# Kernel tuning notes

Hardware: AMD Instinct MI355X
Metric: run time of the kernel (lower is better)

The kernel has to match this reference:

```python
import jax, jax.numpy as jnp
import numpy as np

B, S, D = 1, 2048, 2048
H, G = 32, 8            # n_heads, n_groups
HPG = H // G            # heads per group = 4
HD = D // H             # head_dim = 64


def setup_inputs() -> dict:
    key = jax.random.key(0)
    ks = jax.random.split(key, 5)
    w_scale = 0.02
    return {
        "x":  jax.random.normal(ks[0], (B, S, D), dtype=jnp.float32),
        "Wq": jax.random.normal(ks[1], (D, D), dtype=jnp.float32) * w_scale,
        "bq": jnp.zeros((D,), dtype=jnp.float32),
        "Wk": jax.random.normal(ks[2], (G * HD, D), dtype=jnp.float32) * w_scale,
        "bk": jnp.zeros((G * HD,), dtype=jnp.float32),
        "Wv": jax.random.normal(ks[3], (G * HD, D), dtype=jnp.float32) * w_scale,
        "bv": jnp.zeros((G * HD,), dtype=jnp.float32),
        "Wo": jax.random.normal(ks[4], (D, D), dtype=jnp.float32) * w_scale,
        "bo": jnp.zeros((D,), dtype=jnp.float32),
    }


def reference(x, Wq, bq, Wk, bk, Wv, bv, Wo, bo):
    b, n, _ = x.shape
    # projections (torch Linear: y = x @ W.T + b)
    q = x @ Wq.T + bq                              # [b, n, D]
    k = x @ Wk.T + bk                              # [b, n, G*HD]
    v = x @ Wv.T + bv                              # [b, n, G*HD]
    # q: [b, n, H, HD] -> [b, H, n, HD] -> split heads as (g h): [b, G, HPG, n, HD]
    q = q.reshape(b, n, H, HD).transpose(0, 2, 1, 3).reshape(b, G, HPG, n, HD)
    k = k.reshape(b, n, G, HD).transpose(0, 2, 1, 3)   # [b, G, n, HD]
    v = v.reshape(b, n, G, HD).transpose(0, 2, 1, 3)   # [b, G, n, HD]
    scale = 1.0 / jnp.sqrt(jnp.asarray(HD, dtype=q.dtype))
    attn_score = jnp.einsum('bghnd,bgsd->bghns', q, k) * scale
    attn_prob = jax.nn.softmax(attn_score, axis=-1)
    out = jnp.einsum('bghns,bgsd->bghnd', attn_prob, v)   # [b, G, HPG, n, HD]
    # faithful to original: rearrange 'b g h n d -> b n (h g d)' (h-major, g-minor)
    out = out.transpose(0, 3, 2, 1, 4).reshape(b, n, HPG * G * HD)
    return out @ Wo.T + bo
```

## Files before the change

kernel.cpp:

```cpp
#include <hip/hip_runtime.h>
#include <hip/hip_bf16.h>

constexpr int kS   = 2048;
constexpr int kD   = 2048;
constexpr int kG   = 8;
constexpr int kHD  = 64;
constexpr int kGHD = 512;
constexpr int kNQKV = kD + 2 * kGHD;

constexpr float kQScale = 0.125f * 1.4426950408889634f;

typedef __attribute__((ext_vector_type(8))) _Float16 f16x8;
typedef __attribute__((ext_vector_type(4))) float    f32x4;

__device__ __forceinline__ ushort f2h(float x) {
    return __builtin_bit_cast(ushort, (_Float16)x);
}
__device__ __forceinline__ float h2f(ushort u) {
    return (float)__builtin_bit_cast(_Float16, u);
}
__device__ __forceinline__ float fast_exp2(float x) {
    return __builtin_amdgcn_exp2f(x);
}

__global__ __launch_bounds__(256) void cvt_f16(
    const float* __restrict__ in, ushort* __restrict__ out, int n, float scale)
{
    const int i = (blockIdx.x * 256 + threadIdx.x) * 4;
    if (i >= n) return;
    const float4 x = *(const float4*)&in[i];
    ushort4 o;
    o.x = f2h(x.x * scale); o.y = f2h(x.y * scale);
    o.z = f2h(x.z * scale); o.w = f2h(x.w * scale);
    *(ushort4*)&out[i] = o;
}

__global__ __launch_bounds__(256) void prep_bias(
    const float* __restrict__ bq, const float* __restrict__ bk,
    const float* __restrict__ bv, float* __restrict__ bqkv)
{
    const int i = blockIdx.x * 256 + threadIdx.x;
    if (i < kD)             bqkv[i] = bq[i] * kQScale;
    else if (i < kD + kGHD) bqkv[i] = bk[i - kD];
    else if (i < kNQKV)     bqkv[i] = bv[i - kD - kGHD];
}

__device__ __forceinline__ int xcd_swizzle(int orig, int nwg) {
    const int cpx = nwg >> 3;
    return (orig & 7) * cpx + (orig >> 3);
}

#define GEMM_PRELUDE(Aptr, Bptr)                                              \
    const int bid  = xcd_swizzle(blockIdx.x, gridDim.x);                      \
    const int m0   = (bid / gridX) * 128;                                     \
    const int n0   = (bid % gridX) * 128;                                     \
    const int tid  = threadIdx.x;                                             \
    const int w    = tid >> 6;                                                \
    const int lane = tid & 63;                                                \
    const int wm   = w >> 2;                                                  \
    const int wn   = w & 3;                                                   \
    const int fr   = lane & 15;                                               \
    const int kq   = lane >> 4;                                               \
    const int srow = w * 16 + (lane >> 2);                                    \
    const int sslot = ((lane & 3) ^ ((lane >> 3) & 3)) * 8;                   \
    const ushort* gA = (Aptr) + (size_t)(m0 + srow) * K + sslot;              \
    const ushort* gB = (Bptr) + (size_t)(n0 + srow) * K + sslot;              \
    const int pslot = (kq ^ ((fr >> 1) & 3)) * 8;                             \
    f32x4 acc[4][2];                                                          \
    _Pragma("unroll")                                                         \
    for (int mi = 0; mi < 4; ++mi)                                            \
        _Pragma("unroll")                                                     \
        for (int ni = 0; ni < 2; ++ni) {                                      \
            f32x4 z = {0.f, 0.f, 0.f, 0.f};                                   \
            acc[mi][ni] = z;                                                  \
        }

#define GEMM_STAGE(buf, k0)                                                   \
    do {                                                                      \
        __builtin_amdgcn_global_load_lds(                                     \
            (const __attribute__((address_space(1))) void*)(gA + (k0)),       \
            (__attribute__((address_space(3))) void*)&lds[buf][0][w * 512],   \
            16, 0, 0);                                                        \
        __builtin_amdgcn_global_load_lds(                                     \
            (const __attribute__((address_space(1))) void*)(gB + (k0)),       \
            (__attribute__((address_space(3))) void*)&lds[buf][1][w * 512],   \
            16, 0, 0);                                                        \
    } while (0)

#define GEMM_KLOOP(MFMA_BODY)                                                 \
    GEMM_STAGE(0, 0);                                                         \
    __syncthreads();                                                          \
    int cur = 0;                                                              \
    for (int k0 = 0; k0 < K; k0 += 32) {                                      \
        if (k0 + 32 < K) GEMM_STAGE(cur ^ 1, k0 + 32);                        \
        f16x8 af[4], bf[2];                                                   \
        _Pragma("unroll")                                                     \
        for (int f = 0; f < 4; ++f)                                           \
            af[f] = *(const f16x8*)&lds[cur][0][(wm * 64 + f * 16 + fr) * 32 + pslot]; \
        _Pragma("unroll")                                                     \
        for (int f = 0; f < 2; ++f)                                           \
            bf[f] = *(const f16x8*)&lds[cur][1][(wn * 32 + f * 16 + fr) * 32 + pslot]; \
        __builtin_amdgcn_s_setprio(1);                                        \
        MFMA_BODY                                                             \
        __builtin_amdgcn_s_setprio(0);                                        \
        __syncthreads();                                                      \
        cur ^= 1;                                                             \
    }

__global__ __launch_bounds__(512) void gemm_qkv(
    const ushort* __restrict__ Af, const ushort* __restrict__ Bf,
    const float* __restrict__ bias,
    ushort* __restrict__ qb16, ushort* __restrict__ kb16, ushort* __restrict__ vt16,
    int K, int gridX)
{
    __shared__ ushort lds[2][2][128 * 32];

    GEMM_PRELUDE(Af, Bf)
    GEMM_KLOOP(
        _Pragma("unroll")
        for (int mi = 0; mi < 4; ++mi)
            _Pragma("unroll")
            for (int ni = 0; ni < 2; ++ni)
                acc[mi][ni] = __builtin_amdgcn_mfma_f32_16x16x32_f16(
                    af[mi], bf[ni], acc[mi][ni], 0, 0, 0);
    )

    const int seg = (n0 < kD) ? 0 : (n0 < kD + kGHD) ? 1 : 2;
    #pragma unroll
    for (int ni = 0; ni < 2; ++ni) {
        const int ncol = n0 + wn * 32 + ni * 16 + fr;
        const float bv = bias[ncol];
        #pragma unroll
        for (int mi = 0; mi < 4; ++mi) {
            #pragma unroll
            for (int i = 0; i < 4; ++i) {
                const int row = m0 + wm * 64 + mi * 16 + kq * 4 + i;
                const ushort u = f2h(acc[mi][ni][i] + bv);
                if (seg == 0)      qb16[(size_t)row * kD   + ncol]              = u;
                else if (seg == 1) kb16[(size_t)row * kGHD + (ncol - kD)]       = u;
                else               vt16[(size_t)(ncol - kD - kGHD) * kS + row]  = u;
            }
        }
    }
}

__global__ __launch_bounds__(512) void gemm_o(
    const ushort* __restrict__ Af, const ushort* __restrict__ Bf,
    const float* __restrict__ bias, float* __restrict__ C, int K, int N, int gridX)
{
    __shared__ ushort lds[2][2][128 * 32];

    GEMM_PRELUDE(Af, Bf)
    GEMM_KLOOP(
        _Pragma("unroll")
        for (int mi = 0; mi < 4; ++mi)
            _Pragma("unroll")
            for (int ni = 0; ni < 2; ++ni)
                acc[mi][ni] = __builtin_amdgcn_mfma_f32_16x16x32_f16(
                    af[mi], bf[ni], acc[mi][ni], 0, 0, 0);
    )

    #pragma unroll
    for (int ni = 0; ni < 2; ++ni) {
        const int ncol = n0 + wn * 32 + ni * 16 + fr;
        const float bv = bias[ncol];
        #pragma unroll
        for (int mi = 0; mi < 4; ++mi)
            #pragma unroll
            for (int i = 0; i < 4; ++i) {
                const int row = m0 + wm * 64 + mi * 16 + kq * 4 + i;
                C[(size_t)row * N + ncol] = acc[mi][ni][i] + bv;
            }
    }
}

__global__ __launch_bounds__(512) void gqa_attn_mfma(
    const ushort* __restrict__ qb,
    const ushort* __restrict__ kb,
    const ushort* __restrict__ vt,
    ushort* __restrict__ oh)
{
    __shared__ ushort Kt[2][64 * 64];
    __shared__ ushort Vt[2][64 * 64];
    __shared__ ushort Pt[8][16 * 64];

    const int g    = blockIdx.y;
    const int q0   = blockIdx.x * 32;
    const int tid  = threadIdx.x;
    const int w    = tid >> 6;
    const int lane = tid & 63;
    const int hp   = w & 3;
    const int qh   = w >> 2;
    const int fr   = lane & 15;
    const int lq   = lane >> 4;
    const int h    = g * 4 + hp;
    const int qbase = q0 + qh * 16;

    const int r = w * 8 + (lane >> 3);
    const int s = (lane & 7) ^ (r & 7);

    __builtin_amdgcn_global_load_lds(
        (const __attribute__((address_space(1))) void*)(kb + (size_t)r * kGHD + g * kHD + s * 8),
        (__attribute__((address_space(3))) void*)(Kt[0] + w * 512), 16, 0, 0);
    __builtin_amdgcn_global_load_lds(
        (const __attribute__((address_space(1))) void*)(vt + (size_t)(g * kHD + r) * kS + s * 8),
        (__attribute__((address_space(3))) void*)(Vt[0] + w * 512), 16, 0, 0);

    f16x8 qf[2];
    #pragma unroll
    for (int ks = 0; ks < 2; ++ks)
        qf[ks] = *(const f16x8*)&qb[(size_t)(qbase + fr) * kD + h * kHD + ks * 32 + lq * 8];

    float mrow = -1e30f, lrow = 0.f;

    f32x4 oacc[4];
    #pragma unroll
    for (int ni = 0; ni < 4; ++ni) {
        f32x4 z = {0.f, 0.f, 0.f, 0.f};
        oacc[ni] = z;
    }

    int cur = 0;
    for (int t = 0; t < kS; t += 64) {
        __syncthreads();

        if (t + 64 < kS) {
            __builtin_amdgcn_global_load_lds(
                (const __attribute__((address_space(1))) void*)
                    (kb + (size_t)(t + 64 + r) * kGHD + g * kHD + s * 8),
                (__attribute__((address_space(3))) void*)(Kt[cur ^ 1] + w * 512), 16, 0, 0);
            __builtin_amdgcn_global_load_lds(
                (const __attribute__((address_space(1))) void*)
                    (vt + (size_t)(g * kHD + r) * kS + t + 64 + s * 8),
                (__attribute__((address_space(3))) void*)(Vt[cur ^ 1] + w * 512), 16, 0, 0);
        }

        f32x4 sc[4];
        #pragma unroll
        for (int ni = 0; ni < 4; ++ni) {
            f32x4 z = {0.f, 0.f, 0.f, 0.f};
            sc[ni] = z;
        }
        #pragma unroll
        for (int ks = 0; ks < 2; ++ks) {
            f16x8 kf[4];
            #pragma unroll
            for (int ni = 0; ni < 4; ++ni)
                kf[ni] = *(const f16x8*)&Kt[cur][(ni * 16 + fr) * 64
                                                 + (((ks * 4 + lq) ^ (fr & 7)) * 8)];
            __builtin_amdgcn_s_setprio(1);
            #pragma unroll
            for (int ni = 0; ni < 4; ++ni)
                sc[ni] = __builtin_amdgcn_mfma_f32_16x16x32_f16(
                    kf[ni], qf[ks], sc[ni], 0, 0, 0);
            __builtin_amdgcn_s_setprio(0);
        }

        float mt = sc[0][0];
        #pragma unroll
        for (int ni = 0; ni < 4; ++ni)
            #pragma unroll
            for (int i = 0; i < 4; ++i)
                mt = fmaxf(mt, sc[ni][i]);
        mt = fmaxf(mt, __shfl_xor(mt, 16));
        mt = fmaxf(mt, __shfl_xor(mt, 32));

        if (__any(mt > mrow + 11.5f)) {
            const float mnew = (mt > mrow + 11.5f) ? mt : mrow;
            const float c = fast_exp2(mrow - mnew);
            lrow *= c;
            mrow = mnew;
            #pragma unroll
            for (int i = 0; i < 4; ++i) {
                const float ci = __shfl(c, lq * 4 + i);
                #pragma unroll
                for (int ni = 0; ni < 4; ++ni)
                    oacc[ni][i] *= ci;
            }
        }

        float ps = 0.f;
        #pragma unroll
        for (int ni = 0; ni < 4; ++ni)
            #pragma unroll
            for (int i = 0; i < 4; ++i) {
                const float p = fast_exp2(sc[ni][i] - mrow);
                sc[ni][i] = p;
                ps += p;
            }
        ps += __shfl_xor(ps, 16);
        ps += __shfl_xor(ps, 32);
        lrow += ps;

        #pragma unroll
        for (int ni = 0; ni < 4; ++ni) {
            const int kg0  = ni * 16 + lq * 4;
            const int slot = (kg0 >> 3) ^ (fr & 7);
            ushort4 pk;
            pk.x = f2h(sc[ni][0]); pk.y = f2h(sc[ni][1]);
            pk.z = f2h(sc[ni][2]); pk.w = f2h(sc[ni][3]);
            *(ushort4*)&Pt[w][fr * 64 + slot * 8 + (kg0 & 7)] = pk;
        }

        #pragma unroll
        for (int ks = 0; ks < 2; ++ks) {
            f16x8 pf, vf[4];
            pf = *(const f16x8*)&Pt[w][fr * 64 + (((ks * 4 + lq) ^ (fr & 7)) * 8)];
            #pragma unroll
            for (int ni = 0; ni < 4; ++ni)
                vf[ni] = *(const f16x8*)&Vt[cur][(ni * 16 + fr) * 64
                                                 + (((ks * 4 + lq) ^ (fr & 7)) * 8)];
            __builtin_amdgcn_s_setprio(1);
            #pragma unroll
            for (int ni = 0; ni < 4; ++ni)
                oacc[ni] = __builtin_amdgcn_mfma_f32_16x16x32_f16(
                    pf, vf[ni], oacc[ni], 0, 0, 0);
            __builtin_amdgcn_s_setprio(0);
        }
        cur ^= 1;
    }

    const float inv = 1.f / lrow;
    #pragma unroll
    for (int i = 0; i < 4; ++i) {
        const float invi = __shfl(inv, lq * 4 + i);
        const size_t row = qbase + lq * 4 + i;
        #pragma unroll
        for (int ni = 0; ni < 4; ++ni) {
            const float o = oacc[ni][i] * invi;
            const size_t addr = row * kD + hp * kGHD + g * kHD + ni * 16 + fr;
            oh[addr] = f2h(o);
        }
    }
}

extern "C" void kernel_launch(void* const* d_in, const int* in_sizes, int n_in,
                              void* d_out, int out_size, void* d_ws, size_t ws_size,
                              hipStream_t stream)
{
    const float* x  = (const float*)d_in[0];
    const float* Wq = (const float*)d_in[1];
    const float* bq = (const float*)d_in[2];
    const float* Wk = (const float*)d_in[3];
    const float* bk = (const float*)d_in[4];
    const float* Wv = (const float*)d_in[5];
    const float* bv = (const float*)d_in[6];
    const float* Wo = (const float*)d_in[7];
    const float* bo = (const float*)d_in[8];
    float* out = (float*)d_out;

    char* p = (char*)d_ws;
    ushort* xf    = (ushort*)p; p += (size_t)kS * kD * 2;
    ushort* wqkvf = (ushort*)p; p += (size_t)kNQKV * kD * 2;
    ushort* wof   = (ushort*)p; p += (size_t)kD * kD * 2;
    float*  bqkv  = (float*)p;  p += 16384;
    ushort* qb16  = (ushort*)p; p += (size_t)kS * kD * 2;
    ushort* kb16  = (ushort*)p; p += (size_t)kS * kGHD * 2;
    ushort* vt16  = (ushort*)p; p += (size_t)kGHD * kS * 2;
    ushort* aoh   = (ushort*)p;

    cvt_f16<<<kS * kD / 1024, 256, 0, stream>>>(x, xf, kS * kD, 1.f);
    cvt_f16<<<kD * kD / 1024, 256, 0, stream>>>(Wq, wqkvf, kD * kD, kQScale);
    cvt_f16<<<kGHD * kD / 1024, 256, 0, stream>>>(Wk, wqkvf + (size_t)kD * kD, kGHD * kD, 1.f);
    cvt_f16<<<kGHD * kD / 1024, 256, 0, stream>>>(
        Wv, wqkvf + (size_t)(kD + kGHD) * kD, kGHD * kD, 1.f);
    cvt_f16<<<kD * kD / 1024, 256, 0, stream>>>(Wo, wof, kD * kD, 1.f);
    prep_bias<<<(kNQKV + 255) / 256, 256, 0, stream>>>(bq, bk, bv, bqkv);

    gemm_qkv<<<(kNQKV / 128) * (kS / 128), 512, 0, stream>>>(
        xf, wqkvf, bqkv, qb16, kb16, vt16, kD, kNQKV / 128);

    gqa_attn_mfma<<<dim3(kS / 32, kG), 512, 0, stream>>>(qb16, kb16, vt16, aoh);

    gemm_o<<<(kD / 128) * (kS / 128), 512, 0, stream>>>(
        aoh, wof, bo, out, kD, kD, kD / 128);
}
```

Baseline: 154.0 us.

## Switch attention to 32x32x16 MFMA with register-resident P via permlane32 swap

Attention now runs 4 waves per block, each owning one head and 32 query rows, and uses 32x32x16 MFMA tiles for both QK^T and PV instead of 16x16x32. The probability tile is repacked in registers with cvt_pkrtz plus v_permlane32_swap, which removes the LDS round-trip for P and its staging buffer. Row statistics then need only one cross-lane shuffle, and output stores are vectorized. Halving the threads per block means each wave issues more K/V staging loads and carries more accumulator registers, which may limit occupancy.

```diff
diff --git a/kernel.cpp b/kernel.cpp
--- a/kernel.cpp
+++ b/kernel.cpp
@@ -10,17 +10,20 @@
 
 constexpr float kQScale = 0.125f * 1.4426950408889634f;
 
-typedef __attribute__((ext_vector_type(8))) _Float16 f16x8;
-typedef __attribute__((ext_vector_type(4))) float    f32x4;
+typedef __attribute__((ext_vector_type(8)))  _Float16 f16x8;
+typedef __attribute__((ext_vector_type(4)))  float    f32x4;
+typedef __attribute__((ext_vector_type(16))) float    f32x16;
+typedef __attribute__((ext_vector_type(4)))  unsigned int u32x4;
 
 __device__ __forceinline__ ushort f2h(float x) {
     return __builtin_bit_cast(ushort, (_Float16)x);
 }
-__device__ __forceinline__ float h2f(ushort u) {
-    return (float)__builtin_bit_cast(_Float16, u);
-}
 __device__ __forceinline__ float fast_exp2(float x) {
     return __builtin_amdgcn_exp2f(x);
+}
+__device__ __forceinline__ unsigned int pkrtz(float a, float b) {
+    auto r = __builtin_amdgcn_cvt_pkrtz(a, b);
+    return __builtin_bit_cast(unsigned int, r);
 }
 
 __global__ __launch_bounds__(256) void cvt_f16(
@@ -174,7 +177,7 @@
     }
 }
 
-__global__ __launch_bounds__(512) void gqa_attn_mfma(
+__global__ __launch_bounds__(256) void gqa_attn_mfma(
     const ushort* __restrict__ qb,
     const ushort* __restrict__ kb,
     const ushort* __restrict__ vt,
@@ -182,87 +185,87 @@
 {
     __shared__ ushort Kt[2][64 * 64];
     __shared__ ushort Vt[2][64 * 64];
-    __shared__ ushort Pt[8][16 * 64];
 
     const int g    = blockIdx.y;
     const int q0   = blockIdx.x * 32;
     const int tid  = threadIdx.x;
     const int w    = tid >> 6;
     const int lane = tid & 63;
-    const int hp   = w & 3;
-    const int qh   = w >> 2;
-    const int fr   = lane & 15;
-    const int lq   = lane >> 4;
-    const int h    = g * 4 + hp;
-    const int qbase = q0 + qh * 16;
-
-    const int r = w * 8 + (lane >> 3);
-    const int s = (lane & 7) ^ (r & 7);
-
-    __builtin_amdgcn_global_load_lds(
-        (const __attribute__((address_space(1))) void*)(kb + (size_t)r * kGHD + g * kHD + s * 8),
-        (__attribute__((address_space(3))) void*)(Kt[0] + w * 512), 16, 0, 0);
-    __builtin_amdgcn_global_load_lds(
-        (const __attribute__((address_space(1))) void*)(vt + (size_t)(g * kHD + r) * kS + s * 8),
-        (__attribute__((address_space(3))) void*)(Vt[0] + w * 512), 16, 0, 0);
-
-    f16x8 qf[2];
-    #pragma unroll
-    for (int ks = 0; ks < 2; ++ks)
-        qf[ks] = *(const f16x8*)&qb[(size_t)(qbase + fr) * kD + h * kHD + ks * 32 + lq * 8];
+    const int ql   = lane & 31;
+    const int hi   = lane >> 5;
+    const int h    = g * 4 + w;
+
+    const int r0 = w * 16 + (lane >> 3);
+    const int ss = (lane & 7) ^ (r0 & 7);
+
+#define ATTN_STAGE(buf, t)                                                         \
+    do {                                                                           \
+        __builtin_amdgcn_global_load_lds(                                          \
+            (const __attribute__((address_space(1))) void*)                       \
+                (kb + (size_t)((t) + r0) * kGHD + g * kHD + ss * 8),               \
+            (__attribute__((address_space(3))) void*)(Kt[buf] + (w * 16) * 64),    \
+            16, 0, 0);                                                             \
+        __builtin_amdgcn_global_load_lds(                                          \
+            (const __attribute__((address_space(1))) void*)                       \
+                (kb + (size_t)((t) + r0 + 8) * kGHD + g * kHD + ss * 8),           \
+            (__attribute__((address_space(3))) void*)(Kt[buf] + (w * 16 + 8) * 64),\
+            16, 0, 0);                                                             \
+        __builtin_amdgcn_global_load_lds(                                          \
+            (const __attribute__((address_space(1))) void*)                       \
+                (vt + (size_t)(g * kHD + r0) * kS + (t) + ss * 8),                 \
+            (__attribute__((address_space(3))) void*)(Vt[buf] + (w * 16) * 64),    \
+            16, 0, 0);                                                             \
+        __builtin_amdgcn_global_load_lds(                                          \
+            (const __attribute__((address_space(1))) void*)                       \
+                (vt + (size_t)(g * kHD + r0 + 8) * kS + (t) + ss * 8),             \
+            (__attribute__((address_space(3))) void*)(Vt[buf] + (w * 16 + 8) * 64),\
+            16, 0, 0);                                                             \
+    } while (0)
+
+    ATTN_STAGE(0, 0);
+
+    f16x8 qf[4];
+    #pragma unroll
+    for (int ks = 0; ks < 4; ++ks)
+        qf[ks] = *(const f16x8*)&qb[(size_t)(q0 + ql) * kD + h * kHD + ks * 16 + hi * 8];
 
     float mrow = -1e30f, lrow = 0.f;
-
-    f32x4 oacc[4];
-    #pragma unroll
-    for (int ni = 0; ni < 4; ++ni) {
-        f32x4 z = {0.f, 0.f, 0.f, 0.f};
-        oacc[ni] = z;
-    }
+    f32x16 oacc[2];
+    #pragma unroll
+    for (int db = 0; db < 2; ++db)
+        #pragma unroll
+        for (int r = 0; r < 16; ++r) oacc[db][r] = 0.f;
 
     int cur = 0;
     for (int t = 0; t < kS; t += 64) {
         __syncthreads();
 
-        if (t + 64 < kS) {
-            __builtin_amdgcn_global_load_lds(
-                (const __attribute__((address_space(1))) void*)
-                    (kb + (size_t)(t + 64 + r) * kGHD + g * kHD + s * 8),
-                (__attribute__((address_space(3))) void*)(Kt[cur ^ 1] + w * 512), 16, 0, 0);
-            __builtin_amdgcn_global_load_lds(
-                (const __attribute__((address_space(1))) void*)
-                    (vt + (size_t)(g * kHD + r) * kS + t + 64 + s * 8),
-                (__attribute__((address_space(3))) void*)(Vt[cur ^ 1] + w * 512), 16, 0, 0);
-        }
-
-        f32x4 sc[4];
-        #pragma unroll
-        for (int ni = 0; ni < 4; ++ni) {
-            f32x4 z = {0.f, 0.f, 0.f, 0.f};
-            sc[ni] = z;
-        }
-        #pragma unroll
-        for (int ks = 0; ks < 2; ++ks) {
-            f16x8 kf[4];
-            #pragma unroll
-            for (int ni = 0; ni < 4; ++ni)
-                kf[ni] = *(const f16x8*)&Kt[cur][(ni * 16 + fr) * 64
-                                                 + (((ks * 4 + lq) ^ (fr & 7)) * 8)];
-            __builtin_amdgcn_s_setprio(1);
-            #pragma unroll
-            for (int ni = 0; ni < 4; ++ni)
-                sc[ni] = __builtin_amdgcn_mfma_f32_16x16x32_f16(
-                    kf[ni], qf[ks], sc[ni], 0, 0, 0);
-            __builtin_amdgcn_s_setprio(0);
+        if (t + 64 < kS) ATTN_STAGE(cur ^ 1, t + 64);
+
+        f32x16 sc[2];
+        #pragma unroll
+        for (int kb2 = 0; kb2 < 2; ++kb2)
+            #pragma unroll
+            for (int r = 0; r < 16; ++r) sc[kb2][r] = 0.f;
+
+        #pragma unroll
+        for (int kb2 = 0; kb2 < 2; ++kb2) {
+            #pragma unroll
+            for (int ks = 0; ks < 4; ++ks) {
+                const f16x8 kf = *(const f16x8*)&Kt[cur][(kb2 * 32 + ql) * 64
+                                     + (((2 * ks + hi) ^ (ql & 7)) * 8)];
+                __builtin_amdgcn_s_setprio(1);
+                sc[kb2] = __builtin_amdgcn_mfma_f32_32x32x16_f16(
+                    kf, qf[ks], sc[kb2], 0, 0, 0);
+                __builtin_amdgcn_s_setprio(0);
+            }
         }
 
         float mt = sc[0][0];
         #pragma unroll
-        for (int ni = 0; ni < 4; ++ni)
-            #pragma unroll
-            for (int i = 0; i < 4; ++i)
-                mt = fmaxf(mt, sc[ni][i]);
-        mt = fmaxf(mt, __shfl_xor(mt, 16));
+        for (int kb2 = 0; kb2 < 2; ++kb2)
+            #pragma unroll
+            for (int r = 0; r < 16; ++r) mt = fmaxf(mt, sc[kb2][r]);
         mt = fmaxf(mt, __shfl_xor(mt, 32));
 
         if (__any(mt > mrow + 11.5f)) {
@@ -271,67 +274,66 @@
             lrow *= c;
             mrow = mnew;
             #pragma unroll
-            for (int i = 0; i < 4; ++i) {
-                const float ci = __shfl(c, lq * 4 + i);
+            for (int db = 0; db < 2; ++db)
                 #pragma unroll
-                for (int ni = 0; ni < 4; ++ni)
-                    oacc[ni][i] *= ci;
-            }
+                for (int r = 0; r < 16; ++r) oacc[db][r] *= c;
         }
 
         float ps = 0.f;
         #pragma unroll
-        for (int ni = 0; ni < 4; ++ni)
-            #pragma unroll
-            for (int i = 0; i < 4; ++i) {
-                const float p = fast_exp2(sc[ni][i] - mrow);
-                sc[ni][i] = p;
+        for (int kb2 = 0; kb2 < 2; ++kb2)
+            #pragma unroll
+            for (int r = 0; r < 16; ++r) {
+                const float p = fast_exp2(sc[kb2][r] - mrow);
+                sc[kb2][r] = p;
                 ps += p;
             }
-        ps += __shfl_xor(ps, 16);
         ps += __shfl_xor(ps, 32);
         lrow += ps;
 
         #pragma unroll
-        for (int ni = 0; ni < 4; ++ni) {
-            const int kg0  = ni * 16 + lq * 4;
-            const int slot = (kg0 >> 3) ^ (fr & 7);
-            ushort4 pk;
-            pk.x = f2h(sc[ni][0]); pk.y = f2h(sc[ni][1]);
-            pk.z = f2h(sc[ni][2]); pk.w = f2h(sc[ni][3]);
-            *(ushort4*)&Pt[w][fr * 64 + slot * 8 + (kg0 & 7)] = pk;
-        }
-
-        #pragma unroll
-        for (int ks = 0; ks < 2; ++ks) {
-            f16x8 pf, vf[4];
-            pf = *(const f16x8*)&Pt[w][fr * 64 + (((ks * 4 + lq) ^ (fr & 7)) * 8)];
-            #pragma unroll
-            for (int ni = 0; ni < 4; ++ni)
-                vf[ni] = *(const f16x8*)&Vt[cur][(ni * 16 + fr) * 64
-                                                 + (((ks * 4 + lq) ^ (fr & 7)) * 8)];
-            __builtin_amdgcn_s_setprio(1);
-            #pragma unroll
-            for (int ni = 0; ni < 4; ++ni)
-                oacc[ni] = __builtin_amdgcn_mfma_f32_16x16x32_f16(
-                    pf, vf[ni], oacc[ni], 0, 0, 0);
-            __builtin_amdgcn_s_setprio(0);
+        for (int kb2 = 0; kb2 < 2; ++kb2) {
+            #pragma unroll
+            for (int ks = 0; ks < 2; ++ks) {
+                unsigned int a0 = pkrtz(sc[kb2][8 * ks + 0], sc[kb2][8 * ks + 1]);
+                unsigned int a1 = pkrtz(sc[kb2][8 * ks + 2], sc[kb2][8 * ks + 3]);
+                unsigned int b0 = pkrtz(sc[kb2][8 * ks + 4], sc[kb2][8 * ks + 5]);
+                unsigned int b1 = pkrtz(sc[kb2][8 * ks + 6], sc[kb2][8 * ks + 7]);
+                asm volatile("v_permlane32_swap_b32 %0, %1"
+                             : "+v"(a0), "+v"(b0));
+                asm volatile("v_permlane32_swap_b32 %0, %1"
+                             : "+v"(a1), "+v"(b1));
+                const u32x4 pu = {a0, a1, b0, b1};
+                const f16x8 pf = __builtin_bit_cast(f16x8, pu);
+                #pragma unroll
+                for (int db = 0; db < 2; ++db) {
+                    const f16x8 vf = *(const f16x8*)&Vt[cur][(db * 32 + ql) * 64
+                                         + (((4 * kb2 + 2 * ks + hi) ^ (ql & 7)) * 8)];
+                    __builtin_amdgcn_s_setprio(1);
+                    oacc[db] = __builtin_amdgcn_mfma_f32_32x32x16_f16(
+                        vf, pf, oacc[db], 0, 0, 0);
+                    __builtin_amdgcn_s_setprio(0);
+                }
+            }
         }
         cur ^= 1;
     }
 
     const float inv = 1.f / lrow;
-    #pragma unroll
-    for (int i = 0; i < 4; ++i) {
-        const float invi = __shfl(inv, lq * 4 + i);
-        const size_t row = qbase + lq * 4 + i;
-        #pragma unroll
-        for (int ni = 0; ni < 4; ++ni) {
-            const float o = oacc[ni][i] * invi;
-            const size_t addr = row * kD + hp * kGHD + g * kHD + ni * 16 + fr;
-            oh[addr] = f2h(o);
-        }
-    }
+    const size_t rowbase = (size_t)(q0 + ql) * kD + w * kGHD + g * kHD;
+    #pragma unroll
+    for (int db = 0; db < 2; ++db) {
+        #pragma unroll
+        for (int rr = 0; rr < 4; ++rr) {
+            ushort4 o4;
+            o4.x = f2h(oacc[db][rr * 4 + 0] * inv);
+            o4.y = f2h(oacc[db][rr * 4 + 1] * inv);
+            o4.z = f2h(oacc[db][rr * 4 + 2] * inv);
+            o4.w = f2h(oacc[db][rr * 4 + 3] * inv);
+            *(ushort4*)&oh[rowbase + db * 32 + rr * 8 + hi * 4] = o4;
+        }
+    }
+#undef ATTN_STAGE
 }
 
 extern "C" void kernel_launch(void* const* d_in, const int* in_sizes, int n_in,
@@ -370,7 +372,7 @@
     gemm_qkv<<<(kNQKV / 128) * (kS / 128), 512, 0, stream>>>(
         xf, wqkvf, bqkv, qb16, kb16, vt16, kD, kNQKV / 128);
 
-    gqa_attn_mfma<<<dim3(kS / 32, kG), 512, 0, stream>>>(qb16, kb16, vt16, aoh);
+    gqa_attn_mfma<<<dim3(kS / 32, kG), 256, 0, stream>>>(qb16, kb16, vt16, aoh);
 
     gemm_o<<<(kD / 128) * (kS / 128), 512, 0, stream>>>(
         aoh, wof, bo, out, kD, kD, kD / 128);
```

Measured after the change: 159.4 us. 3.5% more time.
